# Kernel tuning notes

Measured on AMD Instinct MI355X. Metric: run time of the kernel, lower is better.

The kernel has to match this reference:

```python
import jax, jax.numpy as jnp
import numpy as np

B, SQ, SK = 2, 2048, 2048   # batch, n_query, n_memory
D, H, DFF = 1024, 16, 1024  # model dim, heads, ffn dim (must equal D per source constraints)
DH = D // H                 # head dim = 64
NEG = 1e9


def _split_heads(x):
    # (B, S, D) -> (B, H, S, DH)
    b, s, _ = x.shape
    return x.reshape(b, s, H, DH).transpose(0, 2, 1, 3)


def setup_inputs() -> dict:
    key = jax.random.key(0)
    ks = jax.random.split(key, 10)
    s = 0.02
    return {
        "q": jax.random.normal(ks[0], (B, SQ, D), jnp.float32),
        "k": jax.random.normal(ks[1], (B, SK, D), jnp.float32),
        "v": jax.random.normal(ks[2], (B, SK, D), jnp.float32),
        "Win_w": jax.random.normal(ks[3], (DFF, D), jnp.float32) * s,
        "Win_b": jnp.zeros((DFF,), jnp.float32),
        "Wff_w": jax.random.normal(ks[4], (D, DFF), jnp.float32) * s,
        "Wff_b": jnp.zeros((D,), jnp.float32),
        "Wout_w": jax.random.normal(ks[5], (D, D), jnp.float32) * s,
        "Wout_b": jnp.zeros((D,), jnp.float32),
        "attn_mask": jax.random.randint(ks[6], (B, SK), 0, 2, jnp.int32),
    }


def reference(q, k, v, Win_w, Win_b, Wff_w, Wff_b, Wout_w, Wout_b, attn_mask):
    # projections (in_linear; k,v additionally pass through out_linear as in source)
    qh = q @ Win_w.T + Win_b
    kh = (k @ Win_w.T + Win_b) @ Wout_w.T + Wout_b
    vh = (v @ Win_w.T + Win_b) @ Wout_w.T + Wout_b
    qh = qh * (D ** -0.5)

    qh, kh, vh = _split_heads(qh), _split_heads(kh), _split_heads(vh)

    # additive mask bias: 0 where mask==1, -1e9 where mask==0, broadcast over heads/queries
    bias = (attn_mask.astype(jnp.float32) - 1.0) * NEG  # (B, SK)
    scores = jnp.einsum("bhqd,bhkd->bhqk", qh, kh) + bias[:, None, None, :]
    probs = jax.nn.softmax(scores, axis=-1)
    out = jnp.einsum("bhqk,bhkd->bhqd", probs, vh)

    # merge heads: (B, H, SQ, DH) -> (B, SQ, D)
    out = out.transpose(0, 2, 1, 3).reshape(B, SQ, D)

    out = out @ Wff_w.T + Wff_b
    out = out @ Wout_w.T + Wout_b
    return out
```

## Files before the change

kernel.cpp:

```cpp
#include <hip/hip_runtime.h>
#include <cstdint>
#include <cstddef>

using u16 = unsigned short;
using u32 = unsigned int;

typedef __attribute__((ext_vector_type(8))) short short8;
typedef __attribute__((ext_vector_type(4))) float f32x4;

#define MFMA16(a, b, c) __builtin_amdgcn_mfma_f32_16x16x32_bf16((a), (b), (c), 0, 0, 0)

#define QSCALE 0.0450842200f

__device__ __forceinline__ u16 f2bf(float f) {
  u32 u = __float_as_uint(f);
  return (u16)((u + 0x7FFFu + ((u >> 16) & 1u)) >> 16);
}

__device__ __forceinline__ u32 pack_bf16(float a, float b) {
  u32 r;
  asm("v_cvt_pk_bf16_f32 %0, %1, %2" : "=v"(r) : "v"(a), "v"(b));
  return r;
}

__device__ __forceinline__ void gload_lds16(const u16* g, u16* l) {
  __builtin_amdgcn_global_load_lds((const __attribute__((address_space(1))) void*)g,
                                   (__attribute__((address_space(3))) void*)l, 16, 0, 0);
}

__global__ __launch_bounds__(256) void prep_all(
    const float* __restrict__ q, const float* __restrict__ k, const float* __restrict__ v,
    const float* __restrict__ Wout_w, const float* __restrict__ Win_w,
    const float* __restrict__ Wff_w, const float* __restrict__ Win_b,
    const float* __restrict__ Wout_b, u16* __restrict__ X,
    u16* __restrict__ Woutb, u16* __restrict__ Winb,
    u16* __restrict__ WinT, u16* __restrict__ WffT,
    float* __restrict__ bias2, float* __restrict__ bias1f) {
  __shared__ float tile[64][68];
  const int t = threadIdx.x;
  const int bid = blockIdx.x;
  if (bid < 12288) {
    int i4 = bid * 256 + t;
    const float* src = (i4 < 1048576) ? q : (i4 < 2097152) ? k : v;
    int loc = i4 & 1048575;
    float4 w = reinterpret_cast<const float4*>(src)[loc];
    u32 lo = (u32)f2bf(w.x) | ((u32)f2bf(w.y) << 16);
    u32 hi = (u32)f2bf(w.z) | ((u32)f2bf(w.w) << 16);
    reinterpret_cast<uint2*>(X)[i4] = make_uint2(lo, hi);
  } else if (bid < 14336) {
    const int wb = bid - 12288;
    const float* src = wb < 1024 ? Wout_w : Win_w;
    u16* dst = wb < 1024 ? Woutb : Winb;
    const float sc = wb < 1024 ? 1.0f : QSCALE;
    int i = (wb & 1023) * 256 + t;
    float4 vv = reinterpret_cast<const float4*>(src)[i];
    u32 lo = (u32)f2bf(vv.x * sc) | ((u32)f2bf(vv.y * sc) << 16);
    u32 hi = (u32)f2bf(vv.z * sc) | ((u32)f2bf(vv.w * sc) << 16);
    reinterpret_cast<uint2*>(dst)[i] = make_uint2(lo, hi);
  } else if (bid < 14848) {
    const int tb = bid - 14336;
    const float* in = tb < 256 ? Win_w : Wff_w;
    u16* out = tb < 256 ? WinT : WffT;
    const int tix = tb & 255;
    const int bx = (tix >> 4) * 64, by = (tix & 15) * 64;
    const int r = t >> 2, c16 = (t & 3) * 16;
#pragma unroll
    for (int i = 0; i < 4; ++i)
      *reinterpret_cast<float4*>(&tile[r][c16 + i * 4]) =
          *reinterpret_cast<const float4*>(&in[(size_t)(bx + r) * 1024 + by + c16 + i * 4]);
    __syncthreads();
    const int jj = t >> 2, i16 = (t & 3) * 16;
#pragma unroll
    for (int i = 0; i < 4; ++i) {
      uint2 p;
      p.x = (u32)f2bf(tile[i16 + i * 4 + 0][jj]) | ((u32)f2bf(tile[i16 + i * 4 + 1][jj]) << 16);
      p.y = (u32)f2bf(tile[i16 + i * 4 + 2][jj]) | ((u32)f2bf(tile[i16 + i * 4 + 3][jj]) << 16);
      *reinterpret_cast<uint2*>(&out[(size_t)(by + jj) * 1024 + bx + i16 + i * 4]) = p;
    }
  } else if (bid < 15104) {
    const int w = t >> 6, l = t & 63;
    const int j = (bid - 14848) * 4 + w;
    const float4* Wr = reinterpret_cast<const float4*>(Wout_w + (size_t)j * 1024);
    const float4* br = reinterpret_cast<const float4*>(Win_b);
    float s = 0.f;
    for (int i = l; i < 256; i += 64) {
      float4 a = Wr[i], b = br[i];
      s += a.x * b.x + a.y * b.y + a.z * b.z + a.w * b.w;
    }
#pragma unroll
    for (int o = 1; o < 64; o <<= 1) s += __shfl_xor(s, o);
    if (l == 0) bias2[j] = s + Wout_b[j];
  } else {
    float4 vv = reinterpret_cast<const float4*>(Win_b)[t];
    vv.x *= QSCALE; vv.y *= QSCALE; vv.z *= QSCALE; vv.w *= QSCALE;
    reinterpret_cast<float4*>(bias1f)[t] = vv;
  }
}

__global__ __launch_bounds__(256) void bias_comb(const float* __restrict__ W,
                                                 const float* __restrict__ bin,
                                                 const float* __restrict__ badd,
                                                 float* __restrict__ outb) {
  const int w = threadIdx.x >> 6, l = threadIdx.x & 63;
  const int j = blockIdx.x * 4 + w;
  const float4* Wr = reinterpret_cast<const float4*>(W + (size_t)j * 1024);
  const float4* br = reinterpret_cast<const float4*>(bin);
  float s = 0.f;
  for (int i = l; i < 256; i += 64) {
    float4 a = Wr[i], b = br[i];
    s += a.x * b.x + a.y * b.y + a.z * b.z + a.w * b.w;
  }
#pragma unroll
  for (int o = 1; o < 64; o <<= 1) s += __shfl_xor(s, o);
  if (l == 0) outb[j] = s + badd[j];
}

__global__ __launch_bounds__(256) void gemm_w2(const u16* __restrict__ A,
                                               const u16* __restrict__ Bt0,
                                               const u16* __restrict__ Bt1,
                                               u16* __restrict__ C0,
                                               u16* __restrict__ C1) {
  const int bid = blockIdx.x;
  const int xcd = bid & 7, local = bid >> 3;
  const int z = local >> 5;
  const int mt = xcd * 2 + ((local >> 4) & 1);
  const int nt = local & 15;
  const u16* Bt = z ? Bt1 : Bt0;
  u16* C = z ? C1 : C0;
  __shared__ __align__(16) u16 As[2][4096];
  __shared__ __align__(16) u16 Bs[2][4096];
  const int t = threadIdx.x, w = t >> 6, l = t & 63;
  const int l15 = l & 15, l4 = l >> 4;
  const int m0 = mt * 64, n0 = nt * 64;
  f32x4 acc[4] = {};
  const int row0 = t >> 3, cs0 = t & 7;
  const int c0 = cs0 ^ (row0 & 7);
  const int row1 = row0 + 32;
  const int c1 = cs0 ^ (row1 & 7);
  const u16* gA0 = A + (size_t)(m0 + row0) * 1024 + c0 * 8;
  const u16* gA1 = A + (size_t)(m0 + row1) * 1024 + c1 * 8;
  const u16* gB0 = Bt + (size_t)(n0 + row0) * 1024 + c0 * 8;
  const u16* gB1 = Bt + (size_t)(n0 + row1) * 1024 + c1 * 8;
#define W2_STAGE(KK, DST)                             \
  gload_lds16(gA0 + (KK), &As[DST][0] + w * 512);     \
  gload_lds16(gA1 + (KK), &As[DST][2048] + w * 512);  \
  gload_lds16(gB0 + (KK), &Bs[DST][0] + w * 512);     \
  gload_lds16(gB1 + (KK), &Bs[DST][2048] + w * 512);
  W2_STAGE(0, 0)
  for (int step = 0; step < 16; ++step) {
    const int c = step & 1;
    __syncthreads();
    if (step < 15) { W2_STAGE((step + 1) * 64, c ^ 1) }
#pragma unroll
    for (int ks = 0; ks < 2; ++ks) {
      const int cc = ks * 4 + l4;
      short8 bfr = *reinterpret_cast<const short8*>(&Bs[c][(w * 16 + l15) * 64 + ((cc ^ (l15 & 7)) * 8)]);
#pragma unroll
      for (int i = 0; i < 4; ++i) {
        short8 afr = *reinterpret_cast<const short8*>(&As[c][(i * 16 + l15) * 64 + ((cc ^ (l15 & 7)) * 8)]);
        acc[i] = MFMA16(afr, bfr, acc[i]);
      }
    }
  }
#pragma unroll
  for (int i = 0; i < 4; ++i)
#pragma unroll
    for (int j = 0; j < 4; ++j)
      C[(size_t)(m0 + i * 16 + l4 * 4 + j) * 1024 + n0 + w * 16 + l15] = f2bf(acc[i][j]);
}

__global__ __launch_bounds__(256) void proj(const u16* __restrict__ X,
                                            const u16* __restrict__ Winb,
                                            const u16* __restrict__ Wc2,
                                            const float* __restrict__ bias1f,
                                            const float* __restrict__ bias2,
                                            u16* __restrict__ Qh,
                                            u16* __restrict__ Kp,
                                            u16* __restrict__ VT) {
  __shared__ __align__(16) u16 As[2][4096];
  __shared__ __align__(16) u16 Bs[2][4096];
  const int t = threadIdx.x, w = t >> 6, l = t & 63;
  const int l15 = l & 15, l4 = l >> 4;
  const int bid = blockIdx.x;
  const int xcd = bid & 7, local = bid >> 3;
  const int mt = xcd * 12 + (local >> 3);
  const int nt = local & 7;
  const int seg = mt >> 5;
  const int m0 = mt * 128;
  const int n0 = nt * 128;
  const int wr = (w >> 1) * 64, wc = (w & 1) * 64;
  const u16* Bt = seg == 0 ? Winb : Wc2;
  const float* bias = seg == 0 ? bias1f : bias2;

  f32x4 acc[4][4] = {};
  const u16* gA = X + (size_t)(m0 + (t >> 2)) * 1024 + (t & 3) * 8;
  const u16* gB = Bt + (size_t)(n0 + (t >> 2)) * 1024 + (t & 3) * 8;
#define PJ_STAGE(KK, DST)                                   \
  gload_lds16(gA + (KK), &As[DST][0] + w * 512);            \
  gload_lds16(gA + (KK) + 65536, &As[DST][2048] + w * 512); \
  gload_lds16(gB + (KK), &Bs[DST][0] + w * 512);            \
  gload_lds16(gB + (KK) + 65536, &Bs[DST][2048] + w * 512);
  PJ_STAGE(0, 0)
  for (int step = 0; step < 32; ++step) {
    const int c = step & 1;
    __syncthreads();
    if (step < 31) { PJ_STAGE((step + 1) * 32, c ^ 1) }
    short8 af[4], bf[4];
#pragma unroll
    for (int i = 0; i < 4; ++i)
      af[i] = *reinterpret_cast<const short8*>(&As[c][(wr + i * 16 + l15) * 32 + l4 * 8]);
#pragma unroll
    for (int i = 0; i < 4; ++i)
      bf[i] = *reinterpret_cast<const short8*>(&Bs[c][(wc + i * 16 + l15) * 32 + l4 * 8]);
#pragma unroll
    for (int mi = 0; mi < 4; ++mi)
#pragma unroll
      for (int ni = 0; ni < 4; ++ni)
        acc[mi][ni] = MFMA16(af[mi], bf[ni], acc[mi][ni]);
  }

#pragma unroll
  for (int mi = 0; mi < 4; ++mi) {
#pragma unroll
    for (int ni = 0; ni < 4; ++ni) {
      const int col = n0 + wc + ni * 16 + l15;
      const float bv = bias[col];
      const int row0 = m0 + wr + mi * 16 + l4 * 4;
      if (seg == 0) {
#pragma unroll
        for (int j = 0; j < 4; ++j)
          Qh[(size_t)(row0 + j) * 1024 + col] = f2bf(acc[mi][ni][j] + bv);
      } else if (seg == 1) {
#pragma unroll
        for (int j = 0; j < 4; ++j)
          Kp[(size_t)(row0 - 4096 + j) * 1024 + col] = f2bf(acc[mi][ni][j] + bv);
      } else {
        const int r = row0 - 8192;
        const int bb = r >> 11;
        const int sk = r & 2047;
        u32 p0 = (u32)f2bf(acc[mi][ni][0] + bv) | ((u32)f2bf(acc[mi][ni][1] + bv) << 16);
        u32 p1 = (u32)f2bf(acc[mi][ni][2] + bv) | ((u32)f2bf(acc[mi][ni][3] + bv) << 16);
        *reinterpret_cast<uint2*>(VT + ((size_t)(bb * 1024 + col)) * 2048 + sk) = make_uint2(p0, p1);
      }
    }
  }
}

__global__ __launch_bounds__(512) void attn(const u16* __restrict__ Qh,
                                            const u16* __restrict__ Kb,
                                            const u16* __restrict__ VT,
                                            const int* __restrict__ mask,
                                            u16* __restrict__ AO) {
  __shared__ __align__(16) u16 Kt[128 * 64];
  __shared__ __align__(16) u16 Vt[2][64 * 64];
  __shared__ __align__(16) u16 Pw[8 * 16 * 64];
  __shared__ float biasS[2048];
  const int t = threadIdx.x, l = t & 63, w = t >> 6;
  const int l15 = l & 15, l4 = l >> 4;
  const int bid = blockIdx.x;
  const int bh = (bid & 7) * 4 + ((bid >> 3) & 3);
  const int qb = bid >> 5;
  const int b = bh >> 4, h = bh & 15, q0 = qb * 128;

  for (int i = t; i < 2048; i += 512) biasS[i] = mask[b * 2048 + i] ? 0.f : -1.442695e9f;

  short8 qf[2];
  {
    const u16* qp = Qh + (size_t)(b * 2048 + q0 + w * 16 + l15) * 1024 + h * 64 + l4 * 8;
    qf[0] = *reinterpret_cast<const short8*>(qp);
    qf[1] = *reinterpret_cast<const short8*>(qp + 32);
  }
  short8 ones;
#pragma unroll
  for (int i = 0; i < 8; ++i) ones[i] = (short)0x3F80;

  f32x4 acc[4] = {};
  f32x4 accS = {};

  const int rr = t >> 3, cs = t & 7;
  const int ck = cs ^ (rr & 7);
  const u16* gK = Kb + (size_t)(b * 2048 + rr) * 1024 + h * 64 + ck * 8;
  u16* ldsK = Kt + w * 512;
  const u32* gV = reinterpret_cast<const u32*>(VT) + (size_t)(b * 1024 + h * 64 + rr) * 1024 + ck;
  const int pws = w * 1024;

  for (int kt = 0; kt < 2048; kt += 128) {
    const u32* gvt = gV + (kt >> 1);
    u32 A0 = gvt[0], A1 = gvt[8], A2 = gvt[16], A3 = gvt[24];
    u32 B0 = gvt[32], B1 = gvt[40], B2 = gvt[48], B3 = gvt[56];
    __syncthreads();
    gload_lds16(gK + (size_t)kt * 1024, ldsK);
    gload_lds16(gK + (size_t)(kt + 64) * 1024, ldsK + 4096);
    uint4 vv;
    vv.x = (A0 & 0xffffu) | (A1 << 16);
    vv.y = (A2 & 0xffffu) | (A3 << 16);
    vv.z = (A0 >> 16) | (A1 & 0xffff0000u);
    vv.w = (A2 >> 16) | (A3 & 0xffff0000u);
    *reinterpret_cast<uint4*>(&Vt[0][rr * 64 + cs * 8]) = vv;
    vv.x = (B0 & 0xffffu) | (B1 << 16);
    vv.y = (B2 & 0xffffu) | (B3 << 16);
    vv.z = (B0 >> 16) | (B1 & 0xffff0000u);
    vv.w = (B2 >> 16) | (B3 & 0xffff0000u);
    *reinterpret_cast<uint4*>(&Vt[1][rr * 64 + cs * 8]) = vv;
    __syncthreads();

#pragma unroll
    for (int half = 0; half < 2; ++half) {
      const int kb0 = kt + half * 64;
      f32x4 s[4] = {};
      __builtin_amdgcn_s_setprio(1);
#pragma unroll
      for (int ks = 0; ks < 2; ++ks) {
        const int cc = ks * 4 + l4;
#pragma unroll
        for (int n = 0; n < 4; ++n) {
          short8 kb = *reinterpret_cast<const short8*>(
              &Kt[(half * 64 + n * 16 + l15) * 64 + ((cc ^ (l15 & 7)) * 8)]);
          s[n] = MFMA16(qf[ks], kb, s[n]);
        }
      }
      __builtin_amdgcn_s_setprio(0);
#pragma unroll
      for (int n = 0; n < 4; ++n) {
        const float bv = biasS[kb0 + n * 16 + l15];
#pragma unroll
        for (int j = 0; j < 4; ++j) s[n][j] = __builtin_amdgcn_exp2f(s[n][j] + bv);
      }
#pragma unroll
      for (int j = 0; j < 4; ++j) {
        const int r = l4 * 4 + j;
        uint2 pk;
        pk.x = pack_bf16(s[0][j], s[1][j]);
        pk.y = pack_bf16(s[2][j], s[3][j]);
        *reinterpret_cast<uint2*>(
            &Pw[pws + r * 64 + (((l15 >> 1) ^ (r & 7)) * 8) + (l15 & 1) * 4]) = pk;
      }
      __builtin_amdgcn_s_setprio(1);
#pragma unroll
      for (int ks = 0; ks < 2; ++ks) {
        const int cc = ks * 4 + l4;
        short8 pa = *reinterpret_cast<const short8*>(&Pw[pws + l15 * 64 + ((cc ^ (l15 & 7)) * 8)]);
#pragma unroll
        for (int n = 0; n < 4; ++n) {
          short8 vb = *reinterpret_cast<const short8*>(
              &Vt[half][(n * 16 + l15) * 64 + ((cc ^ (l15 & 7)) * 8)]);
          acc[n] = MFMA16(pa, vb, acc[n]);
        }
        accS = MFMA16(pa, ones, accS);
      }
      __builtin_amdgcn_s_setprio(0);
    }
  }

  const size_t orow0 = (size_t)(b * 2048 + q0 + w * 16 + l4 * 4);
#pragma unroll
  for (int j = 0; j < 4; ++j) {
    const float inv = 1.0f / accS[j];
#pragma unroll
    for (int n = 0; n < 4; ++n)
      AO[(orow0 + j) * 1024 + h * 64 + n * 16 + l15] = f2bf(acc[n][j] * inv);
  }
}

__global__ __launch_bounds__(256) void gemm_tail(const u16* __restrict__ A,
                                                 const u16* __restrict__ Bt,
                                                 const float* __restrict__ bias,
                                                 float* __restrict__ C) {
  __shared__ __align__(16) u16 As[2][4096];
  __shared__ __align__(16) u16 Bs[2][2048];
  const int t = threadIdx.x, w = t >> 6, l = t & 63;
  const int l15 = l & 15, l4 = l >> 4;
  const int bid = blockIdx.x;
  const int xcd = bid & 7, local = bid >> 3;
  const int mt = xcd * 4 + (local >> 4);
  const int nt = local & 15;
  const int m0 = mt * 128, n0 = nt * 64;
  const int wr = (w >> 1) * 64, wc = (w & 1) * 32;
  f32x4 acc[4][2] = {};
  const u16* gA = A + (size_t)(m0 + (t >> 2)) * 1024 + (t & 3) * 8;
  const u16* gB = Bt + (size_t)(n0 + (t >> 2)) * 1024 + (t & 3) * 8;
#define TL_STAGE(KK, DST)                                   \
  gload_lds16(gA + (KK), &As[DST][0] + w * 512);            \
  gload_lds16(gA + (KK) + 65536, &As[DST][2048] + w * 512); \
  gload_lds16(gB + (KK), &Bs[DST][0] + w * 512);
  TL_STAGE(0, 0)
  for (int step = 0; step < 32; ++step) {
    const int c = step & 1;
    __syncthreads();
    if (step < 31) { TL_STAGE((step + 1) * 32, c ^ 1) }
    short8 af[4], bf[2];
#pragma unroll
    for (int i = 0; i < 4; ++i)
      af[i] = *reinterpret_cast<const short8*>(&As[c][(wr + i * 16 + l15) * 32 + l4 * 8]);
#pragma unroll
    for (int i = 0; i < 2; ++i)
      bf[i] = *reinterpret_cast<const short8*>(&Bs[c][(wc + i * 16 + l15) * 32 + l4 * 8]);
#pragma unroll
    for (int mi = 0; mi < 4; ++mi)
#pragma unroll
      for (int ni = 0; ni < 2; ++ni)
        acc[mi][ni] = MFMA16(af[mi], bf[ni], acc[mi][ni]);
  }
#pragma unroll
  for (int mi = 0; mi < 4; ++mi) {
#pragma unroll
    for (int ni = 0; ni < 2; ++ni) {
      const int col = n0 + wc + ni * 16 + l15;
      const float bv = bias[col];
      const int row0 = m0 + wr + mi * 16 + l4 * 4;
#pragma unroll
      for (int j = 0; j < 4; ++j)
        C[(size_t)(row0 + j) * 1024 + col] = acc[mi][ni][j] + bv;
    }
  }
}

extern "C" void kernel_launch(void* const* d_in, const int* in_sizes, int n_in,
                              void* d_out, int out_size, void* d_ws, size_t ws_size,
                              hipStream_t stream) {
  const float* q = (const float*)d_in[0];
  const float* k = (const float*)d_in[1];
  const float* v = (const float*)d_in[2];
  const float* Win_w = (const float*)d_in[3];
  const float* Win_b = (const float*)d_in[4];
  const float* Wff_w = (const float*)d_in[5];
  const float* Wff_b = (const float*)d_in[6];
  const float* Wout_w = (const float*)d_in[7];
  const float* Wout_b = (const float*)d_in[8];
  const int* mask = (const int*)d_in[9];
  float* out = (float*)d_out;

  char* ws = (char*)d_ws;
  u16* Xbf = (u16*)ws;
  u16* AO = (u16*)ws;
  float* bias3 = (float*)(ws + 20971520);
  u16* Qh = (u16*)(ws + 25165824);
  u16* WinT = (u16*)(ws + 25165824);
  u16* Woutb = (u16*)(ws + 27262976);
  u16* WffT = (u16*)(ws + 29360128);
  u16* Kproj = (u16*)(ws + 33554432);
  u16* VT = (u16*)(ws + 41943040);
  u16* Wc2 = (u16*)(ws + 50331648);
  u16* Wc3 = (u16*)(ws + 52428800);
  u16* Winb = (u16*)(ws + 54525952);
  float* bias2 = out;
  float* bias1f = out + 1024;

  prep_all<<<15105, 256, 0, stream>>>(q, k, v, Wout_w, Win_w, Wff_w, Win_b, Wout_b,
                                      Xbf, Woutb, Winb, WinT, WffT, bias2, bias1f);
  gemm_w2<<<512, 256, 0, stream>>>(Woutb, WinT, WffT, Wc2, Wc3);
  proj<<<768, 256, 0, stream>>>(Xbf, Winb, Wc2, bias1f, bias2, Qh, Kproj, VT);
  bias_comb<<<256, 256, 0, stream>>>(Wout_w, Wff_b, Wout_b, bias3);
  attn<<<512, 512, 0, stream>>>(Qh, Kproj, VT, mask, AO);
  gemm_tail<<<512, 256, 0, stream>>>(AO, Wc3, bias3, out);
}
```

Before: 150.0 us.

## Split attention over key halves with merge kernel and fold bias init

Splits the attention key dimension into two halves, doubling the grid to 1024 blocks, with each block writing unnormalized bf16 partial outputs and partial row sums. A new merge kernel adds the two partials, normalizes, and also computes the tail bias, replacing the separate bias_comb launch. The mask bias is now loaded as the MFMA accumulator's initial value instead of added after it. This is meant to improve occupancy and load balance across CUs, at the cost of extra global traffic for the partials, one more pass, and extra bf16 rounding of the unnormalized partials.

```diff
diff --git a/kernel.cpp b/kernel.cpp
--- a/kernel.cpp
+++ b/kernel.cpp
@@ -15,6 +15,10 @@
 __device__ __forceinline__ u16 f2bf(float f) {
   u32 u = __float_as_uint(f);
   return (u16)((u + 0x7FFFu + ((u >> 16) & 1u)) >> 16);
+}
+
+__device__ __forceinline__ float bf2f(u32 lo16) {
+  return __uint_as_float(lo16 << 16);
 }
 
 __device__ __forceinline__ u32 pack_bf16(float a, float b) {
@@ -97,24 +101,6 @@
   }
 }
 
-__global__ __launch_bounds__(256) void bias_comb(const float* __restrict__ W,
-                                                 const float* __restrict__ bin,
-                                                 const float* __restrict__ badd,
-                                                 float* __restrict__ outb) {
-  const int w = threadIdx.x >> 6, l = threadIdx.x & 63;
-  const int j = blockIdx.x * 4 + w;
-  const float4* Wr = reinterpret_cast<const float4*>(W + (size_t)j * 1024);
-  const float4* br = reinterpret_cast<const float4*>(bin);
-  float s = 0.f;
-  for (int i = l; i < 256; i += 64) {
-    float4 a = Wr[i], b = br[i];
-    s += a.x * b.x + a.y * b.y + a.z * b.z + a.w * b.w;
-  }
-#pragma unroll
-  for (int o = 1; o < 64; o <<= 1) s += __shfl_xor(s, o);
-  if (l == 0) outb[j] = s + badd[j];
-}
-
 __global__ __launch_bounds__(256) void gemm_w2(const u16* __restrict__ A,
                                                const u16* __restrict__ Bt0,
                                                const u16* __restrict__ Bt1,
@@ -250,19 +236,22 @@
                                             const u16* __restrict__ Kb,
                                             const u16* __restrict__ VT,
                                             const int* __restrict__ mask,
-                                            u16* __restrict__ AO) {
+                                            u16* __restrict__ PP,
+                                            float* __restrict__ S_part) {
   __shared__ __align__(16) u16 Kt[128 * 64];
   __shared__ __align__(16) u16 Vt[2][64 * 64];
   __shared__ __align__(16) u16 Pw[8 * 16 * 64];
-  __shared__ float biasS[2048];
+  __shared__ float biasS[1024];
   const int t = threadIdx.x, l = t & 63, w = t >> 6;
   const int l15 = l & 15, l4 = l >> 4;
   const int bid = blockIdx.x;
   const int bh = (bid & 7) * 4 + ((bid >> 3) & 3);
-  const int qb = bid >> 5;
+  const int rest = bid >> 5;
+  const int qb = rest & 15, kh = rest >> 4;
   const int b = bh >> 4, h = bh & 15, q0 = qb * 128;
-
-  for (int i = t; i < 2048; i += 512) biasS[i] = mask[b * 2048 + i] ? 0.f : -1.442695e9f;
+  const int k0g = kh * 1024;
+
+  for (int i = t; i < 1024; i += 512) biasS[i] = mask[b * 2048 + k0g + i] ? 0.f : -1.442695e9f;
 
   short8 qf[2];
   {
@@ -279,13 +268,13 @@
 
   const int rr = t >> 3, cs = t & 7;
   const int ck = cs ^ (rr & 7);
-  const u16* gK = Kb + (size_t)(b * 2048 + rr) * 1024 + h * 64 + ck * 8;
+  const u16* gK = Kb + (size_t)(b * 2048 + k0g + rr) * 1024 + h * 64 + ck * 8;
   u16* ldsK = Kt + w * 512;
   const u32* gV = reinterpret_cast<const u32*>(VT) + (size_t)(b * 1024 + h * 64 + rr) * 1024 + ck;
   const int pws = w * 1024;
 
-  for (int kt = 0; kt < 2048; kt += 128) {
-    const u32* gvt = gV + (kt >> 1);
+  for (int kt = 0; kt < 1024; kt += 128) {
+    const u32* gvt = gV + ((k0g + kt) >> 1);
     u32 A0 = gvt[0], A1 = gvt[8], A2 = gvt[16], A3 = gvt[24];
     u32 B0 = gvt[32], B1 = gvt[40], B2 = gvt[48], B3 = gvt[56];
     __syncthreads();
@@ -307,7 +296,12 @@
 #pragma unroll
     for (int half = 0; half < 2; ++half) {
       const int kb0 = kt + half * 64;
-      f32x4 s[4] = {};
+      f32x4 s[4];
+#pragma unroll
+      for (int n = 0; n < 4; ++n) {
+        const float bv = biasS[kb0 + n * 16 + l15];
+        s[n][0] = bv; s[n][1] = bv; s[n][2] = bv; s[n][3] = bv;
+      }
       __builtin_amdgcn_s_setprio(1);
 #pragma unroll
       for (int ks = 0; ks < 2; ++ks) {
@@ -321,11 +315,9 @@
       }
       __builtin_amdgcn_s_setprio(0);
 #pragma unroll
-      for (int n = 0; n < 4; ++n) {
-        const float bv = biasS[kb0 + n * 16 + l15];
-#pragma unroll
-        for (int j = 0; j < 4; ++j) s[n][j] = __builtin_amdgcn_exp2f(s[n][j] + bv);
-      }
+      for (int n = 0; n < 4; ++n)
+#pragma unroll
+        for (int j = 0; j < 4; ++j) s[n][j] = __builtin_amdgcn_exp2f(s[n][j]);
 #pragma unroll
       for (int j = 0; j < 4; ++j) {
         const int r = l4 * 4 + j;
@@ -352,13 +344,56 @@
     }
   }
 
+  u16* PPk = PP + (size_t)kh * 4194304;
   const size_t orow0 = (size_t)(b * 2048 + q0 + w * 16 + l4 * 4);
 #pragma unroll
-  for (int j = 0; j < 4; ++j) {
-    const float inv = 1.0f / accS[j];
+  for (int j = 0; j < 4; ++j)
 #pragma unroll
     for (int n = 0; n < 4; ++n)
-      AO[(orow0 + j) * 1024 + h * 64 + n * 16 + l15] = f2bf(acc[n][j] * inv);
+      PPk[(orow0 + j) * 1024 + h * 64 + n * 16 + l15] = f2bf(acc[n][j]);
+  if (l15 == 0) {
+#pragma unroll
+    for (int j = 0; j < 4; ++j) S_part[kh * 4096 + orow0 + j] = accS[j];
+  }
+}
+
+__global__ __launch_bounds__(256) void attn_merge(const u16* __restrict__ PP,
+                                                  const float* __restrict__ S_part,
+                                                  const float* __restrict__ Wout_w,
+                                                  const float* __restrict__ Wff_b,
+                                                  const float* __restrict__ Wout_b,
+                                                  u16* __restrict__ AO,
+                                                  float* __restrict__ bias3) {
+  const int bid = blockIdx.x, t = threadIdx.x;
+  if (bid < 2048) {
+    const size_t e8 = ((size_t)bid * 256 + t) * 8;
+    const int row = (int)(e8 >> 10);
+    const float inv = 1.0f / (S_part[row] + S_part[4096 + row]);
+    uint4 a = *reinterpret_cast<const uint4*>(PP + e8);
+    uint4 c = *reinterpret_cast<const uint4*>(PP + 4194304 + e8);
+    u32 aw[4] = {a.x, a.y, a.z, a.w};
+    u32 cw[4] = {c.x, c.y, c.z, c.w};
+    u32 r[4];
+#pragma unroll
+    for (int i = 0; i < 4; ++i) {
+      float f0 = (bf2f(aw[i] & 0xffffu) + bf2f(cw[i] & 0xffffu)) * inv;
+      float f1 = (bf2f(aw[i] >> 16) + bf2f(cw[i] >> 16)) * inv;
+      r[i] = pack_bf16(f0, f1);
+    }
+    *reinterpret_cast<uint4*>(AO + e8) = make_uint4(r[0], r[1], r[2], r[3]);
+  } else {
+    const int w = t >> 6, l = t & 63;
+    const int j = (bid - 2048) * 4 + w;
+    const float4* Wr = reinterpret_cast<const float4*>(Wout_w + (size_t)j * 1024);
+    const float4* br = reinterpret_cast<const float4*>(Wff_b);
+    float s = 0.f;
+    for (int i = l; i < 256; i += 64) {
+      float4 a = Wr[i], b = br[i];
+      s += a.x * b.x + a.y * b.y + a.z * b.z + a.w * b.w;
+    }
+#pragma unroll
+    for (int o = 1; o < 64; o <<= 1) s += __shfl_xor(s, o);
+    if (l == 0) bias3[j] = s + Wout_b[j];
   }
 }
 
@@ -433,9 +468,10 @@
   char* ws = (char*)d_ws;
   u16* Xbf = (u16*)ws;
   u16* AO = (u16*)ws;
-  float* bias3 = (float*)(ws + 20971520);
+  u16* PP = (u16*)(ws + 8388608);
   u16* Qh = (u16*)(ws + 25165824);
   u16* WinT = (u16*)(ws + 25165824);
+  float* bias3 = (float*)(ws + 25165824);
   u16* Woutb = (u16*)(ws + 27262976);
   u16* WffT = (u16*)(ws + 29360128);
   u16* Kproj = (u16*)(ws + 33554432);
@@ -445,12 +481,13 @@
   u16* Winb = (u16*)(ws + 54525952);
   float* bias2 = out;
   float* bias1f = out + 1024;
+  float* S_part = out + 4096;
 
   prep_all<<<15105, 256, 0, stream>>>(q, k, v, Wout_w, Win_w, Wff_w, Win_b, Wout_b,
                                       Xbf, Woutb, Winb, WinT, WffT, bias2, bias1f);
   gemm_w2<<<512, 256, 0, stream>>>(Woutb, WinT, WffT, Wc2, Wc3);
   proj<<<768, 256, 0, stream>>>(Xbf, Winb, Wc2, bias1f, bias2, Qh, Kproj, VT);
-  bias_comb<<<256, 256, 0, stream>>>(Wout_w, Wff_b, Wout_b, bias3);
-  attn<<<512, 512, 0, stream>>>(Qh, Kproj, VT, mask, AO);
+  attn<<<1024, 512, 0, stream>>>(Qh, Kproj, VT, mask, PP, S_part);
+  attn_merge<<<2304, 256, 0, stream>>>(PP, S_part, Wout_w, Wff_b, Wout_b, AO, bias3);
   gemm_tail<<<512, 256, 0, stream>>>(AO, Wc3, bias3, out);
 }
```

New measurement: 152.9 us. About the same (+1.9%).
